# Kernel tuning notes

Measured on AMD Instinct MI355X. Metric: run time of the kernel, lower is better.

Reference implementation:

```python
import jax, jax.numpy as jnp
import numpy as np

HEAD_DIM = 64


def setup_inputs() -> dict:
    key = jax.random.key(0)
    ks = jax.random.split(key, 5)
    B, T, D = 2, 2048, 1024
    x = jax.random.normal(ks[0], (B, T, D), dtype=jnp.float32)
    # Linear weights stored as [in, out]; scaled like typical init.
    w_qkv = jax.random.normal(ks[1], (D, 3 * D), dtype=jnp.float32) / np.sqrt(D)
    b_qkv = jax.random.normal(ks[2], (3 * D,), dtype=jnp.float32) * 0.02
    w_o = jax.random.normal(ks[3], (D, D), dtype=jnp.float32) / np.sqrt(D)
    b_o = jax.random.normal(ks[4], (D,), dtype=jnp.float32) * 0.02
    return {"x": x, "w_qkv": w_qkv, "b_qkv": b_qkv, "w_o": w_o, "b_o": b_o,
            "window": 256}


def reference(x, w_qkv, b_qkv, w_o, b_o, window):
    B, T, D = x.shape
    H = D // HEAD_DIM
    qkv = x @ w_qkv + b_qkv                      # [B, T, 3D]
    q, k, v = jnp.split(qkv, 3, axis=-1)
    # [B, H, T, hd]
    q = q.reshape(B, T, H, HEAD_DIM).transpose(0, 2, 1, 3)
    k = k.reshape(B, T, H, HEAD_DIM).transpose(0, 2, 1, 3)
    v = v.reshape(B, T, H, HEAD_DIM).transpose(0, 2, 1, 3)
    # Causal band mask: key j valid for query i iff 0 <= i - j <= window.
    idx = jnp.arange(T)
    diff = idx[:, None] - idx[None, :]
    mask = (diff >= 0) & (diff <= window)        # [T, T] bool
    scale = 1.0 / np.sqrt(HEAD_DIM)
    scores = jnp.einsum("bhqd,bhkd->bhqk", q, k) * scale
    scores = jnp.where(mask, scores, -jnp.inf)
    attn = jax.nn.softmax(scores, axis=-1)       # each row has >=1 valid entry
    out = jnp.einsum("bhqk,bhkd->bhqd", attn, v)  # [B, H, T, hd]
    out = out.transpose(0, 2, 1, 3).reshape(B, T, D)
    return out @ w_o + b_o
```

## Files before the change

kernel.cpp:

```cpp
#include <hip/hip_runtime.h>

#define T_SEQ 2048
#define DMODEL 1024
#define NH 16
#define HD 64

typedef unsigned short u16;
typedef short s16;
typedef __attribute__((ext_vector_type(8))) unsigned short u16x8;
typedef __attribute__((ext_vector_type(4))) unsigned short u16x4;
typedef __attribute__((ext_vector_type(8))) short bf16x8;
typedef __attribute__((ext_vector_type(4))) float f32x4;

__device__ __forceinline__ u16 f2bf(float f) {
    union { float f; unsigned u; } v; v.f = f;
    unsigned r = v.u + 0x7fffu + ((v.u >> 16) & 1u);
    return (u16)(r >> 16);
}

__device__ __forceinline__ void gl_lds16(const u16* g, u16* l) {
    __builtin_amdgcn_global_load_lds(
        (const __attribute__((address_space(1))) unsigned int*)g,
        (__attribute__((address_space(3))) unsigned int*)l, 16, 0, 0);
}

__global__ __launch_bounds__(256) void convert_kernel(
    const float* __restrict__ in, u16* __restrict__ out, int n)
{
    int idx = (blockIdx.x * 256 + threadIdx.x) * 4;
    if (idx < n) {
        float4 v = *reinterpret_cast<const float4*>(&in[idx]);
        u16x4 o;
        o.x = f2bf(v.x); o.y = f2bf(v.y); o.z = f2bf(v.z); o.w = f2bf(v.w);
        *reinterpret_cast<u16x4*>(&out[idx]) = o;
    }
}

__global__ __launch_bounds__(256) void transpose_convert_kernel(
    const float* __restrict__ in, u16* __restrict__ out, int K, int N)
{
    __shared__ u16 tile[64][65];
    const int tid = threadIdx.x;
    const int k0 = blockIdx.y * 64, n0 = blockIdx.x * 64;
    const int r  = tid >> 2;
    const int c4 = (tid & 3) * 16;
    #pragma unroll
    for (int i = 0; i < 4; ++i) {
        float4 v = *reinterpret_cast<const float4*>(&in[(size_t)(k0 + r) * N + n0 + c4 + i * 4]);
        tile[c4 + i*4 + 0][r] = f2bf(v.x);
        tile[c4 + i*4 + 1][r] = f2bf(v.y);
        tile[c4 + i*4 + 2][r] = f2bf(v.z);
        tile[c4 + i*4 + 3][r] = f2bf(v.w);
    }
    __syncthreads();
    u16x8 o0, o1;
    #pragma unroll
    for (int i = 0; i < 8; ++i) o0[i] = tile[r][c4 + i];
    #pragma unroll
    for (int i = 0; i < 8; ++i) o1[i] = tile[r][c4 + 8 + i];
    *reinterpret_cast<u16x8*>(&out[(size_t)(n0 + r) * K + k0 + c4])     = o0;
    *reinterpret_cast<u16x8*>(&out[(size_t)(n0 + r) * K + k0 + c4 + 8]) = o1;
}

template<int BM, int BN, bool OUT_BF16>
__global__ __launch_bounds__(256) void gemm_mfma_kernel(
    const u16* __restrict__ A, const u16* __restrict__ BT,
    const float* __restrict__ bias,
    float* __restrict__ C, u16* __restrict__ Cb,
    int M, int N, int K)
{
    constexpr int BK = 64;
    __shared__ __align__(16) u16 As[BM * BK];
    __shared__ __align__(16) u16 Bs[BN * BK];

    const int tid  = threadIdx.x;
    const int wave = tid >> 6, lane = tid & 63;
    const int m0 = blockIdx.y * BM, n0 = blockIdx.x * BN;

    constexpr int WM = BM / 2, WN = BN / 2;
    constexpr int MF = WM / 16, NF = WN / 16;
    const int wm = (wave >> 1) * WM, wn = (wave & 1) * WN;
    const int l15 = lane & 15, l4 = lane >> 4;
    const int l7  = l15 & 7;

    f32x4 acc[MF][NF];
    #pragma unroll
    for (int nf = 0; nf < NF; ++nf) {
        const float bv = bias[n0 + wn + nf * 16 + l15];
        #pragma unroll
        for (int mf = 0; mf < MF; ++mf)
            acc[mf][nf] = (f32x4){bv, bv, bv, bv};
    }

    constexpr int ALOADS = BM / 32;
    constexpr int BLOADS = BN / 32;

    for (int k0 = 0; k0 < K; k0 += BK) {
        __syncthreads();
        #pragma unroll
        for (int i = 0; i < ALOADS; ++i) {
            const int p = tid + i * 256;
            const int r = p >> 3, c = p & 7;
            gl_lds16(&A[(size_t)(m0 + r) * K + k0 + ((c ^ (r & 7)) * 8)], &As[(size_t)p * 8]);
        }
        #pragma unroll
        for (int i = 0; i < BLOADS; ++i) {
            const int p = tid + i * 256;
            const int r = p >> 3, c = p & 7;
            gl_lds16(&BT[(size_t)(n0 + r) * K + k0 + ((c ^ (r & 7)) * 8)], &Bs[(size_t)p * 8]);
        }
        __syncthreads();

        bf16x8 af[MF][2], bfr[NF][2];
        #pragma unroll
        for (int kk = 0; kk < 2; ++kk) {
            const int cc = kk * 4 + l4;
            const int cs = cc ^ l7;
            #pragma unroll
            for (int mf = 0; mf < MF; ++mf)
                af[mf][kk] = *reinterpret_cast<const bf16x8*>(
                    &As[(size_t)((wm + mf * 16 + l15) * 8 + cs) * 8]);
            #pragma unroll
            for (int nf = 0; nf < NF; ++nf)
                bfr[nf][kk] = *reinterpret_cast<const bf16x8*>(
                    &Bs[(size_t)((wn + nf * 16 + l15) * 8 + cs) * 8]);
        }
        #pragma unroll
        for (int kk = 0; kk < 2; ++kk)
            #pragma unroll
            for (int mf = 0; mf < MF; ++mf)
                #pragma unroll
                for (int nf = 0; nf < NF; ++nf)
                    acc[mf][nf] = __builtin_amdgcn_mfma_f32_16x16x32_bf16(
                        af[mf][kk], bfr[nf][kk], acc[mf][nf], 0, 0, 0);
    }

    #pragma unroll
    for (int mf = 0; mf < MF; ++mf)
        #pragma unroll
        for (int nf = 0; nf < NF; ++nf) {
            const int col = n0 + wn + nf * 16 + l15;
            #pragma unroll
            for (int r = 0; r < 4; ++r) {
                const int row = m0 + wm + mf * 16 + l4 * 4 + r;
                if constexpr (OUT_BF16) Cb[(size_t)row * N + col] = f2bf(acc[mf][nf][r]);
                else                    C [(size_t)row * N + col] = acc[mf][nf][r];
            }
        }
}

__global__ __launch_bounds__(256) void swa_mfma_kernel(
    const u16* __restrict__ qkv, u16* __restrict__ out,
    const int* __restrict__ wptr)
{
    const int window = *wptr;
    const int qt = blockIdx.x;
    const int bh = blockIdx.y;
    const int b  = bh >> 4;
    const int h  = bh & (NH - 1);

    const int tid  = threadIdx.x;
    const int wave = tid >> 6, lane = tid & 63;
    const int l15  = lane & 15, l4 = lane >> 4;
    const int hoff = h * HD;

    __shared__ __align__(16) s16 Ks[64 * 64];
    __shared__ __align__(16) s16 Vt[64 * 64];
    __shared__ __align__(16) s16 Ps[64 * 64];

    auto swz = [](int row, int col) { return (row * 64 + col) ^ ((row & 7) << 3); };
    auto vtx = [](int d, int k) { return d * 64 + (((k >> 3) ^ (d >> 3)) & 7) * 8 + (k & 7); };

    const size_t qgrow = (size_t)(b * T_SEQ + qt * 64 + wave * 16 + l15) * (3 * DMODEL) + hoff;
    const bf16x8 qf0 = *reinterpret_cast<const bf16x8*>(&qkv[qgrow + l4 * 8]);
    const bf16x8 qf1 = *reinterpret_cast<const bf16x8*>(&qkv[qgrow + 32 + l4 * 8]);

    f32x4 oacc[4];
    #pragma unroll
    for (int nf = 0; nf < 4; ++nf) oacc[nf] = (f32x4){0.f, 0.f, 0.f, 0.f};
    float m[4] = {-1e30f, -1e30f, -1e30f, -1e30f};
    float l[4] = {0.f, 0.f, 0.f, 0.f};

    const int lo = qt * 64 - window;
    const int cstart = (lo <= 0) ? 0 : (lo >> 6);

    const int kr = tid >> 3;
    const int kc = (tid & 7) * 8;

    for (int c = cstart; c <= qt; ++c) {
        const int j0 = c * 64;
        __syncthreads();
        #pragma unroll
        for (int pass = 0; pass < 2; ++pass) {
            const int row = kr + pass * 32;
            const size_t g = (size_t)(b * T_SEQ + j0 + row) * (3 * DMODEL) + hoff + kc;
            const bf16x8 kv8 = *reinterpret_cast<const bf16x8*>(&qkv[g + DMODEL]);
            const bf16x8 vv8 = *reinterpret_cast<const bf16x8*>(&qkv[g + 2 * DMODEL]);
            *reinterpret_cast<bf16x8*>(&Ks[swz(row, kc)]) = kv8;
            #pragma unroll
            for (int i = 0; i < 8; ++i)
                Vt[vtx(kc + i, row)] = vv8[i];
        }
        __syncthreads();

        f32x4 sacc[4];
        #pragma unroll
        for (int nf = 0; nf < 4; ++nf) sacc[nf] = (f32x4){0.f, 0.f, 0.f, 0.f};
        #pragma unroll
        for (int nf = 0; nf < 4; ++nf) {
            const bf16x8 kf0 = *reinterpret_cast<const bf16x8*>(&Ks[swz(nf * 16 + l15, l4 * 8)]);
            const bf16x8 kf1 = *reinterpret_cast<const bf16x8*>(&Ks[swz(nf * 16 + l15, 32 + l4 * 8)]);
            sacc[nf] = __builtin_amdgcn_mfma_f32_16x16x32_bf16(qf0, kf0, sacc[nf], 0, 0, 0);
            sacc[nf] = __builtin_amdgcn_mfma_f32_16x16x32_bf16(qf1, kf1, sacc[nf], 0, 0, 0);
        }

        float p[4][4];
        #pragma unroll
        for (int r = 0; r < 4; ++r) {
            const int iq = qt * 64 + wave * 16 + l4 * 4 + r;
            float rmax = -1e30f;
            #pragma unroll
            for (int nf = 0; nf < 4; ++nf) {
                const int diff = iq - (j0 + nf * 16 + l15);
                const bool valid = (diff >= 0) && (diff <= window);
                const float s = valid ? sacc[nf][r] * 0.125f : -1e30f;
                p[r][nf] = s;
                rmax = fmaxf(rmax, s);
            }
            rmax = fmaxf(rmax, __shfl_xor(rmax, 1));
            rmax = fmaxf(rmax, __shfl_xor(rmax, 2));
            rmax = fmaxf(rmax, __shfl_xor(rmax, 4));
            rmax = fmaxf(rmax, __shfl_xor(rmax, 8));
            const float mn = fmaxf(m[r], rmax);
            const float rf = __expf(m[r] - mn);
            float rs = 0.f;
            #pragma unroll
            for (int nf = 0; nf < 4; ++nf) {
                const float e = __expf(p[r][nf] - mn);
                p[r][nf] = e;
                rs += e;
            }
            rs += __shfl_xor(rs, 1);
            rs += __shfl_xor(rs, 2);
            rs += __shfl_xor(rs, 4);
            rs += __shfl_xor(rs, 8);
            l[r] = l[r] * rf + rs;
            m[r] = mn;
            #pragma unroll
            for (int nf = 0; nf < 4; ++nf) oacc[nf][r] *= rf;
            #pragma unroll
            for (int nf = 0; nf < 4; ++nf)
                Ps[swz(wave * 16 + l4 * 4 + r, nf * 16 + l15)] = (s16)f2bf(p[r][nf]);
        }
        __syncthreads();

        #pragma unroll
        for (int ks = 0; ks < 2; ++ks) {
            const bf16x8 pa = *reinterpret_cast<const bf16x8*>(&Ps[swz(wave * 16 + l15, ks * 32 + l4 * 8)]);
            #pragma unroll
            for (int nf = 0; nf < 4; ++nf) {
                const bf16x8 vf = *reinterpret_cast<const bf16x8*>(&Vt[vtx(nf * 16 + l15, ks * 32 + l4 * 8)]);
                oacc[nf] = __builtin_amdgcn_mfma_f32_16x16x32_bf16(pa, vf, oacc[nf], 0, 0, 0);
            }
        }
    }

    #pragma unroll
    for (int r = 0; r < 4; ++r) {
        const float inv = 1.f / l[r];
        const size_t orow = (size_t)(b * T_SEQ + qt * 64 + wave * 16 + l4 * 4 + r) * DMODEL + hoff;
        #pragma unroll
        for (int nf = 0; nf < 4; ++nf)
            out[orow + nf * 16 + l15] = f2bf(oacc[nf][r] * inv);
    }
}

extern "C" void kernel_launch(void* const* d_in, const int* in_sizes, int n_in,
                              void* d_out, int out_size, void* d_ws, size_t ws_size,
                              hipStream_t stream) {
    (void)in_sizes; (void)n_in; (void)out_size; (void)ws_size;

    const float* x     = (const float*)d_in[0];
    const float* w_qkv = (const float*)d_in[1];
    const float* b_qkv = (const float*)d_in[2];
    const float* w_o   = (const float*)d_in[3];
    const float* b_o   = (const float*)d_in[4];
    const int*   wnd   = (const int*)d_in[5];

    const int M = 2 * T_SEQ;

    char* w = (char*)d_ws;
    u16* qkvb  = (u16*)(w);
    u16* attb  = (u16*)(w + 24u * 1024 * 1024);
    u16* xb    = (u16*)(w + 32u * 1024 * 1024);
    u16* wqkvT = (u16*)(w + 40u * 1024 * 1024);
    u16* woT   = (u16*)(w + 46u * 1024 * 1024);

    dim3 blk(256);

    convert_kernel<<<dim3(M * DMODEL / 4 / 256), blk, 0, stream>>>(x, xb, M * DMODEL);
    transpose_convert_kernel<<<dim3(3 * DMODEL / 64, DMODEL / 64), blk, 0, stream>>>(
        w_qkv, wqkvT, DMODEL, 3 * DMODEL);
    transpose_convert_kernel<<<dim3(DMODEL / 64, DMODEL / 64), blk, 0, stream>>>(
        w_o, woT, DMODEL, DMODEL);

    gemm_mfma_kernel<128, 128, true><<<dim3(3 * DMODEL / 128, M / 128), blk, 0, stream>>>(
        xb, wqkvT, b_qkv, nullptr, qkvb, M, 3 * DMODEL, DMODEL);

    swa_mfma_kernel<<<dim3(T_SEQ / 64, 2 * NH), blk, 0, stream>>>(qkvb, attb, wnd);

    gemm_mfma_kernel<128, 64, false><<<dim3(DMODEL / 64, M / 128), blk, 0, stream>>>(
        attb, woT, b_o, (float*)d_out, nullptr, M, DMODEL, DMODEL);
}
```

Before: 165.3 us.

## Double-buffer K/V tiles in sliding-window attention and remap GEMM block order

The attention kernel now double-buffers K and V in shared memory. The next K tile is loaded directly into LDS with global_load_lds, and the next V tile is loaded into registers and written transposed after the current PV product, so global loads overlap with compute. This also removes one barrier per iteration. The GEMM kernel remaps workgroup IDs in an XCD-style interleave to improve L2 locality, and the attention kernel gets a min-occupancy hint of 4. The cost is twice the LDS for K and V, extra register pressure from the prefetched V, and a reliance on the async LDS load being complete at the barrier.

```diff
diff --git a/kernel.cpp b/kernel.cpp
--- a/kernel.cpp
+++ b/kernel.cpp
@@ -18,7 +18,7 @@
     return (u16)(r >> 16);
 }
 
-__device__ __forceinline__ void gl_lds16(const u16* g, u16* l) {
+__device__ __forceinline__ void gl_lds16(const void* g, void* l) {
     __builtin_amdgcn_global_load_lds(
         (const __attribute__((address_space(1))) unsigned int*)g,
         (__attribute__((address_space(3))) unsigned int*)l, 16, 0, 0);
@@ -75,7 +75,11 @@
 
     const int tid  = threadIdx.x;
     const int wave = tid >> 6, lane = tid & 63;
-    const int m0 = blockIdx.y * BM, n0 = blockIdx.x * BN;
+
+    const int nwg = gridDim.x * gridDim.y;
+    const int d   = blockIdx.y * gridDim.x + blockIdx.x;
+    const int o   = (d & 7) * (nwg >> 3) + (d >> 3);
+    const int m0 = (o / gridDim.x) * BM, n0 = (o % gridDim.x) * BN;
 
     constexpr int WM = BM / 2, WN = BN / 2;
     constexpr int MF = WM / 16, NF = WN / 16;
@@ -149,7 +153,7 @@
         }
 }
 
-__global__ __launch_bounds__(256) void swa_mfma_kernel(
+__global__ __launch_bounds__(256, 4) void swa_mfma_kernel(
     const u16* __restrict__ qkv, u16* __restrict__ out,
     const int* __restrict__ wptr)
 {
@@ -164,8 +168,8 @@
     const int l15  = lane & 15, l4 = lane >> 4;
     const int hoff = h * HD;
 
-    __shared__ __align__(16) s16 Ks[64 * 64];
-    __shared__ __align__(16) s16 Vt[64 * 64];
+    __shared__ __align__(16) s16 Ks[2][64 * 64];
+    __shared__ __align__(16) s16 Vt[2][64 * 64];
     __shared__ __align__(16) s16 Ps[64 * 64];
 
     auto swz = [](int row, int col) { return (row * 64 + col) ^ ((row & 7) << 3); };
@@ -187,29 +191,52 @@
     const int kr = tid >> 3;
     const int kc = (tid & 7) * 8;
 
+    auto issueK = [&](int c, int buf) {
+        #pragma unroll
+        for (int pass = 0; pass < 2; ++pass) {
+            const int p = tid + pass * 256;
+            const int r = p >> 3, cc = p & 7;
+            const size_t g = (size_t)(b * T_SEQ + c * 64 + r) * (3 * DMODEL)
+                             + DMODEL + hoff + ((cc ^ (r & 7)) * 8);
+            gl_lds16(&qkv[g], &Ks[buf][(size_t)p * 8]);
+        }
+    };
+    auto loadV = [&](int c, bf16x8& v0, bf16x8& v1) {
+        const size_t g0 = (size_t)(b * T_SEQ + c * 64 + kr) * (3 * DMODEL) + 2 * DMODEL + hoff + kc;
+        const size_t g1 = (size_t)(b * T_SEQ + c * 64 + kr + 32) * (3 * DMODEL) + 2 * DMODEL + hoff + kc;
+        v0 = *reinterpret_cast<const bf16x8*>(&qkv[g0]);
+        v1 = *reinterpret_cast<const bf16x8*>(&qkv[g1]);
+    };
+    auto writeV = [&](const bf16x8& v0, const bf16x8& v1, int buf) {
+        #pragma unroll
+        for (int i = 0; i < 8; ++i) Vt[buf][vtx(kc + i, kr)]      = v0[i];
+        #pragma unroll
+        for (int i = 0; i < 8; ++i) Vt[buf][vtx(kc + i, kr + 32)] = v1[i];
+    };
+
+    {
+        issueK(cstart, 0);
+        bf16x8 v0, v1;
+        loadV(cstart, v0, v1);
+        __syncthreads();
+        writeV(v0, v1, 0);
+        __syncthreads();
+    }
+
+    int cur = 0;
     for (int c = cstart; c <= qt; ++c) {
         const int j0 = c * 64;
-        __syncthreads();
-        #pragma unroll
-        for (int pass = 0; pass < 2; ++pass) {
-            const int row = kr + pass * 32;
-            const size_t g = (size_t)(b * T_SEQ + j0 + row) * (3 * DMODEL) + hoff + kc;
-            const bf16x8 kv8 = *reinterpret_cast<const bf16x8*>(&qkv[g + DMODEL]);
-            const bf16x8 vv8 = *reinterpret_cast<const bf16x8*>(&qkv[g + 2 * DMODEL]);
-            *reinterpret_cast<bf16x8*>(&Ks[swz(row, kc)]) = kv8;
-            #pragma unroll
-            for (int i = 0; i < 8; ++i)
-                Vt[vtx(kc + i, row)] = vv8[i];
-        }
-        __syncthreads();
+        bf16x8 nv0, nv1;
+        const bool pre = (c < qt);
+        if (pre) { issueK(c + 1, cur ^ 1); loadV(c + 1, nv0, nv1); }
 
         f32x4 sacc[4];
         #pragma unroll
         for (int nf = 0; nf < 4; ++nf) sacc[nf] = (f32x4){0.f, 0.f, 0.f, 0.f};
         #pragma unroll
         for (int nf = 0; nf < 4; ++nf) {
-            const bf16x8 kf0 = *reinterpret_cast<const bf16x8*>(&Ks[swz(nf * 16 + l15, l4 * 8)]);
-            const bf16x8 kf1 = *reinterpret_cast<const bf16x8*>(&Ks[swz(nf * 16 + l15, 32 + l4 * 8)]);
+            const bf16x8 kf0 = *reinterpret_cast<const bf16x8*>(&Ks[cur][swz(nf * 16 + l15, l4 * 8)]);
+            const bf16x8 kf1 = *reinterpret_cast<const bf16x8*>(&Ks[cur][swz(nf * 16 + l15, 32 + l4 * 8)]);
             sacc[nf] = __builtin_amdgcn_mfma_f32_16x16x32_bf16(qf0, kf0, sacc[nf], 0, 0, 0);
             sacc[nf] = __builtin_amdgcn_mfma_f32_16x16x32_bf16(qf1, kf1, sacc[nf], 0, 0, 0);
         }
@@ -259,10 +286,13 @@
             const bf16x8 pa = *reinterpret_cast<const bf16x8*>(&Ps[swz(wave * 16 + l15, ks * 32 + l4 * 8)]);
             #pragma unroll
             for (int nf = 0; nf < 4; ++nf) {
-                const bf16x8 vf = *reinterpret_cast<const bf16x8*>(&Vt[vtx(nf * 16 + l15, ks * 32 + l4 * 8)]);
+                const bf16x8 vf = *reinterpret_cast<const bf16x8*>(&Vt[cur][vtx(nf * 16 + l15, ks * 32 + l4 * 8)]);
                 oacc[nf] = __builtin_amdgcn_mfma_f32_16x16x32_bf16(pa, vf, oacc[nf], 0, 0, 0);
             }
         }
+        if (pre) writeV(nv0, nv1, cur ^ 1);
+        __syncthreads();
+        cur ^= 1;
     }
 
     #pragma unroll
```

New measurement: 178.7 us. 1.08x slower.

## Merge prep conversions into one launch and use 128-query attention tiles

Applied to the files above, without the earlier changes.

Three conversion kernels (x to bf16, and transposing both weight matrices) are folded into a single prep kernel that dispatches on block index, removing two launches. The sliding-window attention kernel now runs 8 waves per block covering 128 queries, so each staged K/V tile is shared by twice as many query rows. Each wave skips compute for key tiles outside its band, though all waves still join the barriers. This halves the attention grid and adds chunks that only some waves use, which can cost occupancy and add idle barrier time.

```diff
diff --git a/kernel.cpp b/kernel.cpp
--- a/kernel.cpp
+++ b/kernel.cpp
@@ -18,30 +18,45 @@
     return (u16)(r >> 16);
 }
 
-__device__ __forceinline__ void gl_lds16(const u16* g, u16* l) {
+__device__ __forceinline__ void gl_lds16(const void* g, void* l) {
     __builtin_amdgcn_global_load_lds(
         (const __attribute__((address_space(1))) unsigned int*)g,
         (__attribute__((address_space(3))) unsigned int*)l, 16, 0, 0);
 }
 
-__global__ __launch_bounds__(256) void convert_kernel(
-    const float* __restrict__ in, u16* __restrict__ out, int n)
-{
-    int idx = (blockIdx.x * 256 + threadIdx.x) * 4;
-    if (idx < n) {
-        float4 v = *reinterpret_cast<const float4*>(&in[idx]);
-        u16x4 o;
-        o.x = f2bf(v.x); o.y = f2bf(v.y); o.z = f2bf(v.z); o.w = f2bf(v.w);
-        *reinterpret_cast<u16x4*>(&out[idx]) = o;
-    }
-}
-
-__global__ __launch_bounds__(256) void transpose_convert_kernel(
-    const float* __restrict__ in, u16* __restrict__ out, int K, int N)
+#define XCONV_BLOCKS 4096
+#define WQKV_BLOCKS  768
+#define WO_BLOCKS    256
+
+__global__ __launch_bounds__(256) void prep_kernel(
+    const float* __restrict__ x,     u16* __restrict__ xb,
+    const float* __restrict__ wqkv,  u16* __restrict__ wqkvT,
+    const float* __restrict__ wo,    u16* __restrict__ woT)
 {
     __shared__ u16 tile[64][65];
     const int tid = threadIdx.x;
-    const int k0 = blockIdx.y * 64, n0 = blockIdx.x * 64;
+    const int bid = blockIdx.x;
+
+    if (bid < XCONV_BLOCKS) {
+        const int idx = (bid * 256 + tid) * 4;
+        float4 v = *reinterpret_cast<const float4*>(&x[idx]);
+        u16x4 o;
+        o.x = f2bf(v.x); o.y = f2bf(v.y); o.z = f2bf(v.z); o.w = f2bf(v.w);
+        *reinterpret_cast<u16x4*>(&xb[idx]) = o;
+        return;
+    }
+
+    const float* in; u16* out; int K, N, bx, by;
+    if (bid < XCONV_BLOCKS + WQKV_BLOCKS) {
+        const int bi = bid - XCONV_BLOCKS;
+        in = wqkv; out = wqkvT; K = DMODEL; N = 3 * DMODEL;
+        bx = bi % 48; by = bi / 48;
+    } else {
+        const int bi = bid - XCONV_BLOCKS - WQKV_BLOCKS;
+        in = wo; out = woT; K = DMODEL; N = DMODEL;
+        bx = bi % 16; by = bi / 16;
+    }
+    const int k0 = by * 64, n0 = bx * 64;
     const int r  = tid >> 2;
     const int c4 = (tid & 3) * 16;
     #pragma unroll
@@ -149,7 +164,7 @@
         }
 }
 
-__global__ __launch_bounds__(256) void swa_mfma_kernel(
+__global__ __launch_bounds__(512) void swa_mfma_kernel(
     const u16* __restrict__ qkv, u16* __restrict__ out,
     const int* __restrict__ wptr)
 {
@@ -166,12 +181,12 @@
 
     __shared__ __align__(16) s16 Ks[64 * 64];
     __shared__ __align__(16) s16 Vt[64 * 64];
-    __shared__ __align__(16) s16 Ps[64 * 64];
+    __shared__ __align__(16) s16 Ps[128 * 64];
 
     auto swz = [](int row, int col) { return (row * 64 + col) ^ ((row & 7) << 3); };
     auto vtx = [](int d, int k) { return d * 64 + (((k >> 3) ^ (d >> 3)) & 7) * 8 + (k & 7); };
 
-    const size_t qgrow = (size_t)(b * T_SEQ + qt * 64 + wave * 16 + l15) * (3 * DMODEL) + hoff;
+    const size_t qgrow = (size_t)(b * T_SEQ + qt * 128 + wave * 16 + l15) * (3 * DMODEL) + hoff;
     const bf16x8 qf0 = *reinterpret_cast<const bf16x8*>(&qkv[qgrow + l4 * 8]);
     const bf16x8 qf1 = *reinterpret_cast<const bf16x8*>(&qkv[qgrow + 32 + l4 * 8]);
 
@@ -181,86 +196,93 @@
     float m[4] = {-1e30f, -1e30f, -1e30f, -1e30f};
     float l[4] = {0.f, 0.f, 0.f, 0.f};
 
-    const int lo = qt * 64 - window;
+    const int lo = qt * 128 - window;
     const int cstart = (lo <= 0) ? 0 : (lo >> 6);
+    const int cend   = 2 * qt + 1;
 
     const int kr = tid >> 3;
     const int kc = (tid & 7) * 8;
 
-    for (int c = cstart; c <= qt; ++c) {
+    const int q0 = qt * 128 + wave * 16;
+
+    for (int c = cstart; c <= cend; ++c) {
         const int j0 = c * 64;
         __syncthreads();
-        #pragma unroll
-        for (int pass = 0; pass < 2; ++pass) {
-            const int row = kr + pass * 32;
-            const size_t g = (size_t)(b * T_SEQ + j0 + row) * (3 * DMODEL) + hoff + kc;
-            const bf16x8 kv8 = *reinterpret_cast<const bf16x8*>(&qkv[g + DMODEL]);
-            const bf16x8 vv8 = *reinterpret_cast<const bf16x8*>(&qkv[g + 2 * DMODEL]);
-            *reinterpret_cast<bf16x8*>(&Ks[swz(row, kc)]) = kv8;
+        {
+            const size_t g = (size_t)(b * T_SEQ + j0 + kr) * (3 * DMODEL) + DMODEL + hoff + kc;
+            const bf16x8 kv8 = *reinterpret_cast<const bf16x8*>(&qkv[g]);
+            const bf16x8 vv8 = *reinterpret_cast<const bf16x8*>(&qkv[g + DMODEL]);
+            *reinterpret_cast<bf16x8*>(&Ks[swz(kr, kc)]) = kv8;
             #pragma unroll
             for (int i = 0; i < 8; ++i)
-                Vt[vtx(kc + i, row)] = vv8[i];
-        }
-        __syncthreads();
-
-        f32x4 sacc[4];
-        #pragma unroll
-        for (int nf = 0; nf < 4; ++nf) sacc[nf] = (f32x4){0.f, 0.f, 0.f, 0.f};
-        #pragma unroll
-        for (int nf = 0; nf < 4; ++nf) {
-            const bf16x8 kf0 = *reinterpret_cast<const bf16x8*>(&Ks[swz(nf * 16 + l15, l4 * 8)]);
-            const bf16x8 kf1 = *reinterpret_cast<const bf16x8*>(&Ks[swz(nf * 16 + l15, 32 + l4 * 8)]);
-            sacc[nf] = __builtin_amdgcn_mfma_f32_16x16x32_bf16(qf0, kf0, sacc[nf], 0, 0, 0);
-            sacc[nf] = __builtin_amdgcn_mfma_f32_16x16x32_bf16(qf1, kf1, sacc[nf], 0, 0, 0);
-        }
-
-        float p[4][4];
-        #pragma unroll
-        for (int r = 0; r < 4; ++r) {
-            const int iq = qt * 64 + wave * 16 + l4 * 4 + r;
-            float rmax = -1e30f;
+                Vt[vtx(kc + i, kr)] = vv8[i];
+        }
+        __syncthreads();
+
+        const bool active = (j0 <= q0 + 15) && (j0 + 63 >= q0 - window);
+
+        if (active) {
+            f32x4 sacc[4];
+            #pragma unroll
+            for (int nf = 0; nf < 4; ++nf) sacc[nf] = (f32x4){0.f, 0.f, 0.f, 0.f};
             #pragma unroll
             for (int nf = 0; nf < 4; ++nf) {
-                const int diff = iq - (j0 + nf * 16 + l15);
-                const bool valid = (diff >= 0) && (diff <= window);
-                const float s = valid ? sacc[nf][r] * 0.125f : -1e30f;
-                p[r][nf] = s;
-                rmax = fmaxf(rmax, s);
+                const bf16x8 kf0 = *reinterpret_cast<const bf16x8*>(&Ks[swz(nf * 16 + l15, l4 * 8)]);
+                const bf16x8 kf1 = *reinterpret_cast<const bf16x8*>(&Ks[swz(nf * 16 + l15, 32 + l4 * 8)]);
+                sacc[nf] = __builtin_amdgcn_mfma_f32_16x16x32_bf16(qf0, kf0, sacc[nf], 0, 0, 0);
+                sacc[nf] = __builtin_amdgcn_mfma_f32_16x16x32_bf16(qf1, kf1, sacc[nf], 0, 0, 0);
             }
-            rmax = fmaxf(rmax, __shfl_xor(rmax, 1));
-            rmax = fmaxf(rmax, __shfl_xor(rmax, 2));
-            rmax = fmaxf(rmax, __shfl_xor(rmax, 4));
-            rmax = fmaxf(rmax, __shfl_xor(rmax, 8));
-            const float mn = fmaxf(m[r], rmax);
-            const float rf = __expf(m[r] - mn);
-            float rs = 0.f;
-            #pragma unroll
-            for (int nf = 0; nf < 4; ++nf) {
-                const float e = __expf(p[r][nf] - mn);
-                p[r][nf] = e;
-                rs += e;
+
+            float p[4][4];
+            #pragma unroll
+            for (int r = 0; r < 4; ++r) {
+                const int iq = q0 + l4 * 4 + r;
+                float rmax = -1e30f;
+                #pragma unroll
+                for (int nf = 0; nf < 4; ++nf) {
+                    const int diff = iq - (j0 + nf * 16 + l15);
+                    const bool valid = (diff >= 0) && (diff <= window);
+                    const float s = valid ? sacc[nf][r] * 0.125f : -1e30f;
+                    p[r][nf] = s;
+                    rmax = fmaxf(rmax, s);
+                }
+                rmax = fmaxf(rmax, __shfl_xor(rmax, 1));
+                rmax = fmaxf(rmax, __shfl_xor(rmax, 2));
+                rmax = fmaxf(rmax, __shfl_xor(rmax, 4));
+                rmax = fmaxf(rmax, __shfl_xor(rmax, 8));
+                const float mn = fmaxf(m[r], rmax);
+                const float rf = __expf(m[r] - mn);
+                float rs = 0.f;
+                #pragma unroll
+                for (int nf = 0; nf < 4; ++nf) {
+                    const float e = __expf(p[r][nf] - mn);
+                    p[r][nf] = e;
+                    rs += e;
+                }
+                rs += __shfl_xor(rs, 1);
+                rs += __shfl_xor(rs, 2);
+                rs += __shfl_xor(rs, 4);
+                rs += __shfl_xor(rs, 8);
+                l[r] = l[r] * rf + rs;
+                m[r] = mn;
+                #pragma unroll
+                for (int nf = 0; nf < 4; ++nf) oacc[nf][r] *= rf;
+                #pragma unroll
+                for (int nf = 0; nf < 4; ++nf)
+                    Ps[swz(wave * 16 + l4 * 4 + r, nf * 16 + l15)] = (s16)f2bf(p[r][nf]);
             }
-            rs += __shfl_xor(rs, 1);
-            rs += __shfl_xor(rs, 2);
-            rs += __shfl_xor(rs, 4);
-            rs += __shfl_xor(rs, 8);
-            l[r] = l[r] * rf + rs;
-            m[r] = mn;
-            #pragma unroll
-            for (int nf = 0; nf < 4; ++nf) oacc[nf][r] *= rf;
-            #pragma unroll
-            for (int nf = 0; nf < 4; ++nf)
-                Ps[swz(wave * 16 + l4 * 4 + r, nf * 16 + l15)] = (s16)f2bf(p[r][nf]);
-        }
-        __syncthreads();
-
-        #pragma unroll
-        for (int ks = 0; ks < 2; ++ks) {
-            const bf16x8 pa = *reinterpret_cast<const bf16x8*>(&Ps[swz(wave * 16 + l15, ks * 32 + l4 * 8)]);
-            #pragma unroll
-            for (int nf = 0; nf < 4; ++nf) {
-                const bf16x8 vf = *reinterpret_cast<const bf16x8*>(&Vt[vtx(nf * 16 + l15, ks * 32 + l4 * 8)]);
-                oacc[nf] = __builtin_amdgcn_mfma_f32_16x16x32_bf16(pa, vf, oacc[nf], 0, 0, 0);
+        }
+        __syncthreads();
+
+        if (active) {
+            #pragma unroll
+            for (int ks = 0; ks < 2; ++ks) {
+                const bf16x8 pa = *reinterpret_cast<const bf16x8*>(&Ps[swz(wave * 16 + l15, ks * 32 + l4 * 8)]);
+                #pragma unroll
+                for (int nf = 0; nf < 4; ++nf) {
+                    const bf16x8 vf = *reinterpret_cast<const bf16x8*>(&Vt[vtx(nf * 16 + l15, ks * 32 + l4 * 8)]);
+                    oacc[nf] = __builtin_amdgcn_mfma_f32_16x16x32_bf16(pa, vf, oacc[nf], 0, 0, 0);
+                }
             }
         }
     }
@@ -268,7 +290,7 @@
     #pragma unroll
     for (int r = 0; r < 4; ++r) {
         const float inv = 1.f / l[r];
-        const size_t orow = (size_t)(b * T_SEQ + qt * 64 + wave * 16 + l4 * 4 + r) * DMODEL + hoff;
+        const size_t orow = (size_t)(b * T_SEQ + qt * 128 + wave * 16 + l4 * 4 + r) * DMODEL + hoff;
         #pragma unroll
         for (int nf = 0; nf < 4; ++nf)
             out[orow + nf * 16 + l15] = f2bf(oacc[nf][r] * inv);
@@ -296,19 +318,14 @@
     u16* wqkvT = (u16*)(w + 40u * 1024 * 1024);
     u16* woT   = (u16*)(w + 46u * 1024 * 1024);
 
-    dim3 blk(256);
-
-    convert_kernel<<<dim3(M * DMODEL / 4 / 256), blk, 0, stream>>>(x, xb, M * DMODEL);
-    transpose_convert_kernel<<<dim3(3 * DMODEL / 64, DMODEL / 64), blk, 0, stream>>>(
-        w_qkv, wqkvT, DMODEL, 3 * DMODEL);
-    transpose_convert_kernel<<<dim3(DMODEL / 64, DMODEL / 64), blk, 0, stream>>>(
-        w_o, woT, DMODEL, DMODEL);
-
-    gemm_mfma_kernel<128, 128, true><<<dim3(3 * DMODEL / 128, M / 128), blk, 0, stream>>>(
+    prep_kernel<<<dim3(XCONV_BLOCKS + WQKV_BLOCKS + WO_BLOCKS), dim3(256), 0, stream>>>(
+        x, xb, w_qkv, wqkvT, w_o, woT);
+
+    gemm_mfma_kernel<128, 128, true><<<dim3(3 * DMODEL / 128, M / 128), dim3(256), 0, stream>>>(
         xb, wqkvT, b_qkv, nullptr, qkvb, M, 3 * DMODEL, DMODEL);
 
-    swa_mfma_kernel<<<dim3(T_SEQ / 64, 2 * NH), blk, 0, stream>>>(qkvb, attb, wnd);
-
-    gemm_mfma_kernel<128, 64, false><<<dim3(DMODEL / 64, M / 128), blk, 0, stream>>>(
+    swa_mfma_kernel<<<dim3(T_SEQ / 128, 2 * NH), dim3(512), 0, stream>>>(qkvb, attb, wnd);
+
+    gemm_mfma_kernel<128, 64, false><<<dim3(DMODEL / 64, M / 128), dim3(256), 0, stream>>>(
         attb, woT, b_o, (float*)d_out, nullptr, M, DMODEL, DMODEL);
 }
```

Measured after the change: 165.1 us. Within noise of the previous version (-0.1%).
